# Optimization experiments

Measured on AMD Instinct MI355X. Metric: run time of the kernel, lower is better.

The kernel has to match this reference:

```python
import jax, jax.numpy as jnp
import numpy as np

H = 16          # num_heads
DK = 64         # k_dim_head
DV = 64         # v_dim_head
DIM = 1024      # model dim (= H*DK = H*DV)


def _split_heads(x, h):
    # ... T (H d) -> ... H T d
    x = x.reshape(x.shape[:-1] + (h, -1))
    return jnp.swapaxes(x, -2, -3)


def _merge_heads(x):
    # ... H T d -> ... T (H d)
    x = jnp.swapaxes(x, -2, -3)
    return x.reshape(x.shape[:-2] + (-1,))


def setup_inputs() -> dict:
    key = jax.random.key(0)
    ks = jax.random.split(key, 8)
    B, T = 2, 2048
    q = jax.random.normal(ks[0], (B, T, DIM), dtype=jnp.float32)
    k = jax.random.normal(ks[1], (B, T, DIM), dtype=jnp.float32)
    v = jax.random.normal(ks[2], (B, T, DIM), dtype=jnp.float32)
    # causal boolean mask [T, T] (True = attend)
    mask = jnp.tril(jnp.ones((T, T), dtype=bool))
    s = 1.0 / np.sqrt(DIM)
    # weights stored as [in, out] so projection is x @ W (== torch Linear, no bias)
    Wq = jax.random.normal(ks[3], (DIM, H * DK), dtype=jnp.float32) * s
    Wk = jax.random.normal(ks[4], (DIM, H * DK), dtype=jnp.float32) * s
    Wv = jax.random.normal(ks[5], (DIM, H * DV), dtype=jnp.float32) * s
    Wo = jax.random.normal(ks[6], (H * DV, DIM), dtype=jnp.float32) * s
    return {"q": q, "k": k, "v": v, "mask": mask,
            "Wq": Wq, "Wk": Wk, "Wv": Wv, "Wo": Wo}


def reference(q, k, v, mask, Wq, Wk, Wv, Wo):
    q_i = _split_heads(q @ Wq, H)                       # ... H T dk
    k_i = _split_heads(k @ Wk, H)                       # ... H T dk
    v_i = _split_heads(v @ Wv, H)                       # ... H T dv
    s_qk = jnp.einsum('...hik,...hjk->...hij', q_i, k_i) / jnp.sqrt(
        jnp.asarray(DK, dtype=q_i.dtype))               # ... H T T
    neg = -jnp.finfo(s_qk.dtype).max
    s_qk = jnp.where(mask, s_qk, neg)
    attn = jax.nn.softmax(s_qk, axis=-1)
    vals = jnp.einsum('...hij,...hjv->...hiv', attn, v_i)
    return _merge_heads(vals) @ Wo                      # ... T out_dim
```

## Files before the change

### kernel.cpp

```cpp
#include <hip/hip_runtime.h>
#include <hip/hip_bf16.h>
#include <stdint.h>

#define T_SEQ  2048
#define DMODEL 1024
#define NBATCH 2
#define NHEAD  16
#define DHEAD  64
#define MTOT   (NBATCH * T_SEQ)

typedef __attribute__((ext_vector_type(8))) short short8_t;
typedef __attribute__((ext_vector_type(4))) float f32x4;
typedef __attribute__((ext_vector_type(16))) float f32x16;
typedef __attribute__((ext_vector_type(2))) __bf16 bhalf2_t;
typedef __attribute__((ext_vector_type(4))) uint32_t uint4_t;

typedef const __attribute__((address_space(1))) void* gas_t;
typedef __attribute__((address_space(3))) void* las_t;

__device__ __forceinline__ ushort f2bf(float f) {
    return __builtin_bit_cast(unsigned short, (__bf16)f);
}
__device__ __forceinline__ uint32_t pk_bf16(float a, float b) {
    bhalf2_t t; t[0] = (__bf16)a; t[1] = (__bf16)b;
    return __builtin_bit_cast(uint32_t, t);
}

template <int B>
__device__ __forceinline__ short8_t pack8(const f32x16 &s) {
    uint4_t u;
    u[0] = pk_bf16(s[B + 0], s[B + 1]);
    u[1] = pk_bf16(s[B + 2], s[B + 3]);
    u[2] = pk_bf16(s[B + 4], s[B + 5]);
    u[3] = pk_bf16(s[B + 6], s[B + 7]);
    return __builtin_bit_cast(short8_t, u);
}

__global__ __launch_bounds__(256) void convert_qkv_kernel(
        const float* __restrict__ q, const float* __restrict__ k,
        const float* __restrict__ v, ushort* __restrict__ outb) {
    const size_t per = (size_t)MTOT * DMODEL / 4;
    size_t idx = (size_t)blockIdx.x * 256 + threadIdx.x;
    int t = (int)(idx / per);
    size_t i = idx - (size_t)t * per;
    const float4* src = (const float4*)(t == 0 ? q : (t == 1 ? k : v));
    float4 val = src[i];
    uint2 o;
    o.x = pk_bf16(val.x, val.y);
    o.y = pk_bf16(val.z, val.w);
    ((uint2*)outb)[(size_t)t * per + i] = o;
}

__global__ __launch_bounds__(256) void convw_kernel(
        const float* __restrict__ Wq, const float* __restrict__ Wk,
        const float* __restrict__ Wv, const float* __restrict__ Wo,
        ushort* __restrict__ wt) {
    __shared__ float tile[32][33];
    int z = blockIdx.z;
    const float* W = z == 0 ? Wq : z == 1 ? Wk : z == 2 ? Wv : Wo;
    const float sc = (z == 0) ? 0.18033688011f : 1.0f;
    ushort* out = wt + (size_t)z * DMODEL * DMODEL;
    int tx = threadIdx.x, ty = threadIdx.y;
    int k0 = blockIdx.x * 32, n0 = blockIdx.y * 32;
    #pragma unroll
    for (int i = 0; i < 4; i++)
        tile[ty + i * 8][tx] = W[(size_t)(k0 + ty + i * 8) * DMODEL + n0 + tx];
    __syncthreads();
    #pragma unroll
    for (int i = 0; i < 4; i++)
        out[(size_t)(n0 + ty + i * 8) * DMODEL + k0 + tx] = f2bf(tile[tx][ty + i * 8] * sc);
}

template <bool OUT_F32>
__global__ __launch_bounds__(256, 2) void gemm_bt_kernel(
        const ushort* __restrict__ Aall, const ushort* __restrict__ Btall,
        void* __restrict__ Call, int M, int N, int K) {
    const ushort* A  = Aall  + (size_t)blockIdx.z * M * K;
    const ushort* Bt = Btall + (size_t)blockIdx.z * N * K;

    __shared__ ushort As[128 * 32];
    __shared__ ushort Bs[128 * 32];

    const int tid  = threadIdx.x;
    const int lane = tid & 63;
    const int wid  = tid >> 6;
    const int wr = wid >> 1, wc = wid & 1;
    const int m_base = blockIdx.x * 128;
    const int n_base = blockIdx.y * 128;

    f32x4 acc[4][4] = {};

    const int srow = lane >> 2;
    const int scol = (lane & 3) * 8;

    for (int kk = 0; kk < K; kk += 32) {
        __syncthreads();
        #pragma unroll
        for (int i = 0; i < 2; i++) {
            int c = wid * 2 + i;
            const ushort* ga = A  + (size_t)(m_base + c * 16 + srow) * K + kk + scol;
            const ushort* gb = Bt + (size_t)(n_base + c * 16 + srow) * K + kk + scol;
            __builtin_amdgcn_global_load_lds((gas_t)ga, (las_t)(As + c * 512), 16, 0, 0);
            __builtin_amdgcn_global_load_lds((gas_t)gb, (las_t)(Bs + c * 512), 16, 0, 0);
        }
        __syncthreads();
        short8_t a[4], b[4];
        #pragma unroll
        for (int mt = 0; mt < 4; mt++)
            a[mt] = *(const short8_t*)(As + (wr * 64 + mt * 16 + (lane & 15)) * 32 + (lane >> 4) * 8);
        #pragma unroll
        for (int nt = 0; nt < 4; nt++)
            b[nt] = *(const short8_t*)(Bs + (wc * 64 + nt * 16 + (lane & 15)) * 32 + (lane >> 4) * 8);
        #pragma unroll
        for (int mt = 0; mt < 4; mt++)
            #pragma unroll
            for (int nt = 0; nt < 4; nt++)
                acc[mt][nt] = __builtin_amdgcn_mfma_f32_16x16x32_bf16(a[mt], b[nt], acc[mt][nt], 0, 0, 0);
    }

    const int row0 = m_base + wr * 64 + (lane >> 4) * 4;
    const int col0 = n_base + wc * 64 + (lane & 15);
    if constexpr (OUT_F32) {
        float* C = (float*)Call + (size_t)blockIdx.z * M * N;
        #pragma unroll
        for (int mt = 0; mt < 4; mt++)
            #pragma unroll
            for (int nt = 0; nt < 4; nt++)
                #pragma unroll
                for (int r = 0; r < 4; r++)
                    C[(size_t)(row0 + mt * 16 + r) * N + col0 + nt * 16] = acc[mt][nt][r];
    } else {
        ushort* C = (ushort*)Call + (size_t)blockIdx.z * M * N;
        #pragma unroll
        for (int mt = 0; mt < 4; mt++)
            #pragma unroll
            for (int nt = 0; nt < 4; nt++)
                #pragma unroll
                for (int r = 0; r < 4; r++)
                    C[(size_t)(row0 + mt * 16 + r) * N + col0 + nt * 16] = f2bf(acc[mt][nt][r]);
    }
}

__global__ __launch_bounds__(128, 2) void attn_kernel(
        const ushort* __restrict__ Qp, const ushort* __restrict__ Kp,
        const ushort* __restrict__ Vp, ushort* __restrict__ Op) {
    __shared__ __attribute__((aligned(16))) ushort Ksh[2][64 * 72];
    __shared__ __attribute__((aligned(16))) ushort Vts[2][64 * 72];

    const int tid = threadIdx.x, lane = tid & 63, w = tid >> 6;
    const int m31 = lane & 31, hi = lane >> 5;
    const int bh = blockIdx.y;
    const int b = bh >> 4, h = bh & 15;

    const ushort* Qb = Qp + (size_t)(b * T_SEQ) * DMODEL + h * DHEAD;
    const ushort* Kb = Kp + (size_t)(b * T_SEQ) * DMODEL + h * DHEAD;
    const ushort* Vb = Vp + (size_t)(b * T_SEQ) * DMODEL + h * DHEAD;
    ushort* Ob = Op + (size_t)(b * T_SEQ) * DMODEL + h * DHEAD;

    const int qi = 31 - (int)blockIdx.x;
    const int nt = qi + 1;
    const int q0 = qi * 64;
    const int q0w = q0 + w * 32;
    const int qg = q0w + m31;

    const int kr = tid >> 1, kc64 = (tid & 1) * 32;
    const int kvp = tid & 31, dvs = tid >> 5;
    const int lp = kvp & 7, q2 = lp >> 1;
    const int q2p = ((q2 & 1) << 1) | (q2 >> 1);
    const int kvc = (kvp & ~7) | (q2p << 1) | (lp & 1);

    short8_t kreg[4], vreg[4];
    auto LOADKV = [&](int kv0) {
        #pragma unroll
        for (int j = 0; j < 4; j++)
            kreg[j] = *(const short8_t*)(Kb + (size_t)(kv0 + kr) * DMODEL + kc64 + j * 8);
        const ushort* vsrc = Vb + (size_t)(kv0 + kvp * 2) * DMODEL + dvs * 16;
        vreg[0] = *(const short8_t*)(vsrc);
        vreg[1] = *(const short8_t*)(vsrc + 8);
        vreg[2] = *(const short8_t*)(vsrc + DMODEL);
        vreg[3] = *(const short8_t*)(vsrc + DMODEL + 8);
    };
    auto WRITEKV = [&](int buf) {
        #pragma unroll
        for (int j = 0; j < 4; j++)
            *(short8_t*)(&Ksh[buf][kr * 72 + kc64 + j * 8]) = kreg[j];
        #pragma unroll
        for (int c = 0; c < 2; c++) {
            uint4_t a = __builtin_bit_cast(uint4_t, vreg[c]);
            uint4_t o = __builtin_bit_cast(uint4_t, vreg[2 + c]);
            #pragma unroll
            for (int j = 0; j < 4; j++) {
                int d0 = dvs * 16 + c * 8 + 2 * j;
                *(uint32_t*)(&Vts[buf][(d0 + 0) * 72 + kvc * 2]) =
                    __builtin_amdgcn_perm(o[j], a[j], 0x05040100u);
                *(uint32_t*)(&Vts[buf][(d0 + 1) * 72 + kvc * 2]) =
                    __builtin_amdgcn_perm(o[j], a[j], 0x07060302u);
            }
        }
    };

    short8_t qf[4];
    #pragma unroll
    for (int dkc = 0; dkc < 4; dkc++)
        qf[dkc] = *(const short8_t*)(Qb + (size_t)(q0w + m31) * DMODEL + dkc * 16 + hi * 8);

    f32x16 acc0 = {}, acc1 = {};
    float mrun = -1e30f, lrun = 0.f;

    LOADKV(0);
    WRITEKV(0);
    LOADKV(64);

    for (int t = 0; t < nt; ++t) {
        const int kv0 = t * 64;
        const int cur = t & 1;
        const bool need_mask = (t == nt - 1);

        __syncthreads();
        if (t + 1 < nt) {
            WRITEKV(cur ^ 1);
            if (t + 2 < nt) LOADKV((t + 2) * 64);
        }

        f32x16 s0 = {}, s1 = {};
        __builtin_amdgcn_s_setprio(1);
        #pragma unroll
        for (int dkc = 0; dkc < 4; dkc++) {
            short8_t kf0 = *(const short8_t*)(&Ksh[cur][(m31) * 72 + dkc * 16 + hi * 8]);
            short8_t kf1 = *(const short8_t*)(&Ksh[cur][(32 + m31) * 72 + dkc * 16 + hi * 8]);
            s0 = __builtin_amdgcn_mfma_f32_32x32x16_bf16(kf0, qf[dkc], s0, 0, 0, 0);
            s1 = __builtin_amdgcn_mfma_f32_32x32x16_bf16(kf1, qf[dkc], s1, 0, 0, 0);
        }
        __builtin_amdgcn_s_setprio(0);

        if (need_mask) {
            const int kvb = kv0 + 4 * hi;
            #pragma unroll
            for (int r = 0; r < 16; r++) {
                int kvl = (r & 3) + 8 * (r >> 2);
                if (kvb + kvl      > qg) s0[r] = -1e30f;
                if (kvb + kvl + 32 > qg) s1[r] = -1e30f;
            }
        }

        float tm[16];
        #pragma unroll
        for (int r = 0; r < 16; r++) tm[r] = fmaxf(s0[r], s1[r]);
        #pragma unroll
        for (int st = 8; st >= 1; st >>= 1)
            #pragma unroll
            for (int i = 0; i < st; i++) tm[i] = fmaxf(tm[i], tm[i + st]);
        float pmax = fmaxf(tm[0], __shfl_xor(tm[0], 32));

        if (!__all(pmax <= mrun + 8.f)) {
            float mnew = fmaxf(mrun, pmax);
            float fac = exp2f(mrun - mnew);
            mrun = mnew;
            lrun *= fac;
            #pragma unroll
            for (int r = 0; r < 16; r++) {
                float fr = __shfl(fac, (r & 3) + 8 * (r >> 2) + 4 * hi);
                acc0[r] *= fr; acc1[r] *= fr;
            }
        }

        float ps[16];
        #pragma unroll
        for (int r = 0; r < 16; r++) {
            s0[r] = exp2f(s0[r] - mrun);
            s1[r] = exp2f(s1[r] - mrun);
            ps[r] = s0[r] + s1[r];
        }
        #pragma unroll
        for (int st = 8; st >= 1; st >>= 1)
            #pragma unroll
            for (int i = 0; i < st; i++) ps[i] += ps[i + st];
        lrun += ps[0] + __shfl_xor(ps[0], 32);

        short8_t pa[4];
        pa[0] = pack8<0>(s0);
        pa[1] = pack8<8>(s0);
        pa[2] = pack8<0>(s1);
        pa[3] = pack8<8>(s1);
        __builtin_amdgcn_s_setprio(1);
        #pragma unroll
        for (int ks = 0; ks < 4; ks++) {
            short8_t vf0 = *(const short8_t*)(&Vts[cur][(m31) * 72 + ks * 16 + hi * 8]);
            short8_t vf1 = *(const short8_t*)(&Vts[cur][(32 + m31) * 72 + ks * 16 + hi * 8]);
            acc0 = __builtin_amdgcn_mfma_f32_32x32x16_bf16(pa[ks], vf0, acc0, 0, 0, 0);
            acc1 = __builtin_amdgcn_mfma_f32_32x32x16_bf16(pa[ks], vf1, acc1, 0, 0, 0);
        }
        __builtin_amdgcn_s_setprio(0);
    }

    float linv = __builtin_amdgcn_rcpf(lrun);
    #pragma unroll
    for (int r = 0; r < 16; r++) {
        int ql = (r & 3) + 8 * (r >> 2) + 4 * hi;
        float li = __shfl(linv, ql);
        ushort* orow = Ob + (size_t)(q0w + ql) * DMODEL + m31;
        orow[0]  = f2bf(acc0[r] * li);
        orow[32] = f2bf(acc1[r] * li);
    }
}

extern "C" void kernel_launch(void* const* d_in, const int* in_sizes, int n_in,
                              void* d_out, int out_size, void* d_ws, size_t ws_size,
                              hipStream_t stream) {
    (void)in_sizes; (void)n_in; (void)out_size; (void)ws_size;
    const float* q  = (const float*)d_in[0];
    const float* k  = (const float*)d_in[1];
    const float* v  = (const float*)d_in[2];
    const float* Wq = (const float*)d_in[4];
    const float* Wk = (const float*)d_in[5];
    const float* Wv = (const float*)d_in[6];
    const float* Wo = (const float*)d_in[7];

    ushort* ws = (ushort*)d_ws;
    const size_t MK = (size_t)MTOT * DMODEL;
    const size_t NK = (size_t)DMODEL * DMODEL;
    ushort* qkvb = ws;
    ushort* wt   = ws + 3 * MK;
    ushort* qkvp = ws + 3 * MK + 4 * NK;
    ushort* Op   = ws;

    convert_qkv_kernel<<<dim3(12288), dim3(256), 0, stream>>>(q, k, v, qkvb);
    convw_kernel<<<dim3(32, 32, 4), dim3(32, 8), 0, stream>>>(Wq, Wk, Wv, Wo, wt);
    gemm_bt_kernel<false><<<dim3(32, 8, 3), dim3(256), 0, stream>>>(qkvb, wt, (void*)qkvp,
                                                                    MTOT, DMODEL, DMODEL);
    attn_kernel<<<dim3(32, 32), dim3(128), 0, stream>>>(qkvp, qkvp + MK, qkvp + 2 * MK, Op);
    gemm_bt_kernel<true><<<dim3(32, 8, 1), dim3(256), 0, stream>>>(Op, wt + 3 * NK, d_out,
                                                                   MTOT, DMODEL, DMODEL);
}
```

Before: 149.2 us.

## Pair causal query tiles per block to balance attention workload

Each attention block now handles two query tiles, qa and 31-qa, back to back, so every block processes exactly 33 KV tiles instead of a varying 1 to 32. The grid shrinks from 32x32 to 16x32 blocks, and the KV prefetch pipeline continues across the switch between the two query tiles. This targets the tail imbalance of causal attention, where blocks with many KV tiles finish late. In exchange there are half as many blocks to fill the GPU (512 blocks of 128 threads), plus an extra Q reload and output write in the middle of the loop.

```diff
diff --git a/kernel.cpp b/kernel.cpp
--- a/kernel.cpp
+++ b/kernel.cpp
@@ -157,11 +157,8 @@
     const ushort* Vb = Vp + (size_t)(b * T_SEQ) * DMODEL + h * DHEAD;
     ushort* Ob = Op + (size_t)(b * T_SEQ) * DMODEL + h * DHEAD;
 
-    const int qi = 31 - (int)blockIdx.x;
-    const int nt = qi + 1;
-    const int q0 = qi * 64;
-    const int q0w = q0 + w * 32;
-    const int qg = q0w + m31;
+    const int qa = blockIdx.x;
+    const int na = qa + 1;
 
     const int kr = tid >> 1, kc64 = (tid & 1) * 32;
     const int kvp = tid & 31, dvs = tid >> 5;
@@ -199,6 +196,7 @@
         }
     };
 
+    int qi = qa, q0w = qi * 64 + w * 32, qg = q0w + m31;
     short8_t qf[4];
     #pragma unroll
     for (int dkc = 0; dkc < 4; dkc++)
@@ -207,19 +205,42 @@
     f32x16 acc0 = {}, acc1 = {};
     float mrun = -1e30f, lrun = 0.f;
 
-    LOADKV(0);
+    auto WRITE_O = [&]() {
+        float linv = __builtin_amdgcn_rcpf(lrun);
+        #pragma unroll
+        for (int r = 0; r < 16; r++) {
+            int ql = (r & 3) + 8 * (r >> 2) + 4 * hi;
+            float li = __shfl(linv, ql);
+            ushort* orow = Ob + (size_t)(q0w + ql) * DMODEL + m31;
+            orow[0]  = f2bf(acc0[r] * li);
+            orow[32] = f2bf(acc1[r] * li);
+        }
+    };
+    auto TILE = [&](int t) { return (t < na) ? t : t - na; };
+
+    LOADKV(TILE(0) * 64);
     WRITEKV(0);
-    LOADKV(64);
-
-    for (int t = 0; t < nt; ++t) {
+    LOADKV(TILE(1) * 64);
+
+    for (int tt = 0; tt < 33; ++tt) {
+        if (tt == na) {
+            WRITE_O();
+            acc0 = f32x16{}; acc1 = f32x16{};
+            mrun = -1e30f; lrun = 0.f;
+            qi = 31 - qa; q0w = qi * 64 + w * 32; qg = q0w + m31;
+            #pragma unroll
+            for (int dkc = 0; dkc < 4; dkc++)
+                qf[dkc] = *(const short8_t*)(Qb + (size_t)(q0w + m31) * DMODEL + dkc * 16 + hi * 8);
+        }
+        const int t = TILE(tt);
         const int kv0 = t * 64;
-        const int cur = t & 1;
-        const bool need_mask = (t == nt - 1);
+        const int cur = tt & 1;
+        const bool need_mask = (t == qi);
 
         __syncthreads();
-        if (t + 1 < nt) {
+        if (tt + 1 < 33) {
             WRITEKV(cur ^ 1);
-            if (t + 2 < nt) LOADKV((t + 2) * 64);
+            if (tt + 2 < 33) LOADKV(TILE(tt + 2) * 64);
         }
 
         f32x16 s0 = {}, s1 = {};
@@ -292,16 +313,7 @@
         }
         __builtin_amdgcn_s_setprio(0);
     }
-
-    float linv = __builtin_amdgcn_rcpf(lrun);
-    #pragma unroll
-    for (int r = 0; r < 16; r++) {
-        int ql = (r & 3) + 8 * (r >> 2) + 4 * hi;
-        float li = __shfl(linv, ql);
-        ushort* orow = Ob + (size_t)(q0w + ql) * DMODEL + m31;
-        orow[0]  = f2bf(acc0[r] * li);
-        orow[32] = f2bf(acc1[r] * li);
-    }
+    WRITE_O();
 }
 
 extern "C" void kernel_launch(void* const* d_in, const int* in_sizes, int n_in,
@@ -328,7 +340,7 @@
     convw_kernel<<<dim3(32, 32, 4), dim3(32, 8), 0, stream>>>(Wq, Wk, Wv, Wo, wt);
     gemm_bt_kernel<false><<<dim3(32, 8, 3), dim3(256), 0, stream>>>(qkvb, wt, (void*)qkvp,
                                                                     MTOT, DMODEL, DMODEL);
-    attn_kernel<<<dim3(32, 32), dim3(128), 0, stream>>>(qkvp, qkvp + MK, qkvp + 2 * MK, Op);
+    attn_kernel<<<dim3(16, 32), dim3(128), 0, stream>>>(qkvp, qkvp + MK, qkvp + 2 * MK, Op);
     gemm_bt_kernel<true><<<dim3(32, 8, 1), dim3(256), 0, stream>>>(Op, wt + 3 * NK, d_out,
                                                                    MTOT, DMODEL, DMODEL);
 }
```

After: 146.2 us. -2.0%, faster.

## Split attention into single-wave blocks with balanced causal scheduling

Applied to the files above, without the earlier changes.

The attention kernel changes from 128-thread blocks (two waves sharing a 64-row query tile) to 64-thread single-wave blocks, each owning 32 query rows, for 2048 blocks. Block ids map to query tiles so consecutive blocks pair short and long causal rows, balancing work. Since only one wave uses the shared tiles, the LDS double buffer and __syncthreads are dropped: the next K/V tile is loaded into registers during compute and written to LDS after the PV MFMAs. In exchange, each wave loads full K/V tiles on its own, doubling global and LDS traffic per query row, and register pressure rises.

```diff
diff --git a/kernel.cpp b/kernel.cpp
--- a/kernel.cpp
+++ b/kernel.cpp
@@ -141,15 +141,20 @@
     }
 }
 
-__global__ __launch_bounds__(128, 2) void attn_kernel(
+__global__ __launch_bounds__(64, 2) void attn_kernel(
         const ushort* __restrict__ Qp, const ushort* __restrict__ Kp,
         const ushort* __restrict__ Vp, ushort* __restrict__ Op) {
-    __shared__ __attribute__((aligned(16))) ushort Ksh[2][64 * 72];
-    __shared__ __attribute__((aligned(16))) ushort Vts[2][64 * 72];
-
-    const int tid = threadIdx.x, lane = tid & 63, w = tid >> 6;
+    __shared__ __attribute__((aligned(16))) ushort Ksh[64 * 72];
+    __shared__ __attribute__((aligned(16))) ushort Vts[64 * 72];
+
+    const int lane = threadIdx.x;
     const int m31 = lane & 31, hi = lane >> 5;
-    const int bh = blockIdx.y;
+
+    const int id = (int)blockIdx.x;
+    const int low = id & 255, k8 = id >> 8;
+    const int bh = low >> 3;
+    const int u = ((k8 >> 1) << 3) | (low & 7);
+    const int qb = (k8 & 1) ? 63 - u : u;
     const int b = bh >> 4, h = bh & 15;
 
     const ushort* Qb = Qp + (size_t)(b * T_SEQ) * DMODEL + h * DHEAD;
@@ -157,44 +162,43 @@
     const ushort* Vb = Vp + (size_t)(b * T_SEQ) * DMODEL + h * DHEAD;
     ushort* Ob = Op + (size_t)(b * T_SEQ) * DMODEL + h * DHEAD;
 
-    const int qi = 31 - (int)blockIdx.x;
-    const int nt = qi + 1;
-    const int q0 = qi * 64;
-    const int q0w = q0 + w * 32;
+    const int nt = (qb >> 1) + 1;
+    const int q0w = qb * 32;
     const int qg = q0w + m31;
 
-    const int kr = tid >> 1, kc64 = (tid & 1) * 32;
-    const int kvp = tid & 31, dvs = tid >> 5;
+    const int kr8 = lane >> 3, kc8 = (lane & 7) * 8;
+    const int kvp = lane & 31, dvh = lane >> 5;
     const int lp = kvp & 7, q2 = lp >> 1;
     const int q2p = ((q2 & 1) << 1) | (q2 >> 1);
     const int kvc = (kvp & ~7) | (q2p << 1) | (lp & 1);
 
-    short8_t kreg[4], vreg[4];
+    short8_t kreg[8], vreg[8];
     auto LOADKV = [&](int kv0) {
         #pragma unroll
-        for (int j = 0; j < 4; j++)
-            kreg[j] = *(const short8_t*)(Kb + (size_t)(kv0 + kr) * DMODEL + kc64 + j * 8);
-        const ushort* vsrc = Vb + (size_t)(kv0 + kvp * 2) * DMODEL + dvs * 16;
-        vreg[0] = *(const short8_t*)(vsrc);
-        vreg[1] = *(const short8_t*)(vsrc + 8);
-        vreg[2] = *(const short8_t*)(vsrc + DMODEL);
-        vreg[3] = *(const short8_t*)(vsrc + DMODEL + 8);
+        for (int i = 0; i < 8; i++)
+            kreg[i] = *(const short8_t*)(Kb + (size_t)(kv0 + kr8 + 8 * i) * DMODEL + kc8);
+        const ushort* vsrc = Vb + (size_t)(kv0 + 2 * kvp) * DMODEL + dvh * 32;
+        #pragma unroll
+        for (int j = 0; j < 4; j++) {
+            vreg[j]     = *(const short8_t*)(vsrc + j * 8);
+            vreg[4 + j] = *(const short8_t*)(vsrc + DMODEL + j * 8);
+        }
     };
-    auto WRITEKV = [&](int buf) {
-        #pragma unroll
-        for (int j = 0; j < 4; j++)
-            *(short8_t*)(&Ksh[buf][kr * 72 + kc64 + j * 8]) = kreg[j];
-        #pragma unroll
-        for (int c = 0; c < 2; c++) {
-            uint4_t a = __builtin_bit_cast(uint4_t, vreg[c]);
-            uint4_t o = __builtin_bit_cast(uint4_t, vreg[2 + c]);
-            #pragma unroll
-            for (int j = 0; j < 4; j++) {
-                int d0 = dvs * 16 + c * 8 + 2 * j;
-                *(uint32_t*)(&Vts[buf][(d0 + 0) * 72 + kvc * 2]) =
-                    __builtin_amdgcn_perm(o[j], a[j], 0x05040100u);
-                *(uint32_t*)(&Vts[buf][(d0 + 1) * 72 + kvc * 2]) =
-                    __builtin_amdgcn_perm(o[j], a[j], 0x07060302u);
+    auto WRITEKV = [&]() {
+        #pragma unroll
+        for (int i = 0; i < 8; i++)
+            *(short8_t*)(&Ksh[(kr8 + 8 * i) * 72 + kc8]) = kreg[i];
+        #pragma unroll
+        for (int j = 0; j < 4; j++) {
+            uint4_t a = __builtin_bit_cast(uint4_t, vreg[j]);
+            uint4_t o = __builtin_bit_cast(uint4_t, vreg[4 + j]);
+            #pragma unroll
+            for (int jj = 0; jj < 4; jj++) {
+                int d0 = dvh * 32 + j * 8 + 2 * jj;
+                *(uint32_t*)(&Vts[(d0 + 0) * 72 + kvc * 2]) =
+                    __builtin_amdgcn_perm(o[jj], a[jj], 0x05040100u);
+                *(uint32_t*)(&Vts[(d0 + 1) * 72 + kvc * 2]) =
+                    __builtin_amdgcn_perm(o[jj], a[jj], 0x07060302u);
             }
         }
     };
@@ -208,26 +212,20 @@
     float mrun = -1e30f, lrun = 0.f;
 
     LOADKV(0);
-    WRITEKV(0);
-    LOADKV(64);
+    WRITEKV();
 
     for (int t = 0; t < nt; ++t) {
         const int kv0 = t * 64;
-        const int cur = t & 1;
         const bool need_mask = (t == nt - 1);
 
-        __syncthreads();
-        if (t + 1 < nt) {
-            WRITEKV(cur ^ 1);
-            if (t + 2 < nt) LOADKV((t + 2) * 64);
-        }
+        if (t + 1 < nt) LOADKV((t + 1) * 64);
 
         f32x16 s0 = {}, s1 = {};
         __builtin_amdgcn_s_setprio(1);
         #pragma unroll
         for (int dkc = 0; dkc < 4; dkc++) {
-            short8_t kf0 = *(const short8_t*)(&Ksh[cur][(m31) * 72 + dkc * 16 + hi * 8]);
-            short8_t kf1 = *(const short8_t*)(&Ksh[cur][(32 + m31) * 72 + dkc * 16 + hi * 8]);
+            short8_t kf0 = *(const short8_t*)(&Ksh[(m31) * 72 + dkc * 16 + hi * 8]);
+            short8_t kf1 = *(const short8_t*)(&Ksh[(32 + m31) * 72 + dkc * 16 + hi * 8]);
             s0 = __builtin_amdgcn_mfma_f32_32x32x16_bf16(kf0, qf[dkc], s0, 0, 0, 0);
             s1 = __builtin_amdgcn_mfma_f32_32x32x16_bf16(kf1, qf[dkc], s1, 0, 0, 0);
         }
@@ -285,12 +283,14 @@
         __builtin_amdgcn_s_setprio(1);
         #pragma unroll
         for (int ks = 0; ks < 4; ks++) {
-            short8_t vf0 = *(const short8_t*)(&Vts[cur][(m31) * 72 + ks * 16 + hi * 8]);
-            short8_t vf1 = *(const short8_t*)(&Vts[cur][(32 + m31) * 72 + ks * 16 + hi * 8]);
+            short8_t vf0 = *(const short8_t*)(&Vts[(m31) * 72 + ks * 16 + hi * 8]);
+            short8_t vf1 = *(const short8_t*)(&Vts[(32 + m31) * 72 + ks * 16 + hi * 8]);
             acc0 = __builtin_amdgcn_mfma_f32_32x32x16_bf16(pa[ks], vf0, acc0, 0, 0, 0);
             acc1 = __builtin_amdgcn_mfma_f32_32x32x16_bf16(pa[ks], vf1, acc1, 0, 0, 0);
         }
         __builtin_amdgcn_s_setprio(0);
+
+        if (t + 1 < nt) WRITEKV();
     }
 
     float linv = __builtin_amdgcn_rcpf(lrun);
@@ -328,7 +328,7 @@
     convw_kernel<<<dim3(32, 32, 4), dim3(32, 8), 0, stream>>>(Wq, Wk, Wv, Wo, wt);
     gemm_bt_kernel<false><<<dim3(32, 8, 3), dim3(256), 0, stream>>>(qkvb, wt, (void*)qkvp,
                                                                     MTOT, DMODEL, DMODEL);
-    attn_kernel<<<dim3(32, 32), dim3(128), 0, stream>>>(qkvp, qkvp + MK, qkvp + 2 * MK, Op);
+    attn_kernel<<<dim3(2048), dim3(64), 0, stream>>>(qkvp, qkvp + MK, qkvp + 2 * MK, Op);
     gemm_bt_kernel<true><<<dim3(32, 8, 1), dim3(256), 0, stream>>>(Op, wt + 3 * NK, d_out,
                                                                    MTOT, DMODEL, DMODEL);
 }
```

After: 148.1 us. Within noise of the previous version (-0.7%).

## Use 128-row query tiles with 4 waves and atomic work-queue scheduling in attention

Applied to the files above, without the earlier changes.

Attention blocks now process 128 query rows with four waves sharing each K/V shared-memory tile, halving global K/V traffic per query. Blocks fetch work units from an atomic counter in largest-first order to balance the causal triangle, and a small kernel resets the counter. Waves whose rows end before the last tile skip compute on that tile but still take part in the loads and barriers. The cost is one more launch and some idle wave time on the diagonal tiles.

```diff
diff --git a/kernel.cpp b/kernel.cpp
--- a/kernel.cpp
+++ b/kernel.cpp
@@ -71,6 +71,10 @@
         out[(size_t)(n0 + ty + i * 8) * DMODEL + k0 + tx] = f2bf(tile[tx][ty + i * 8] * sc);
 }
 
+__global__ void zero_ctr_kernel(uint32_t* ctr) {
+    if (threadIdx.x == 0 && blockIdx.x == 0) *ctr = 0u;
+}
+
 template <bool OUT_F32>
 __global__ __launch_bounds__(256, 2) void gemm_bt_kernel(
         const ushort* __restrict__ Aall, const ushort* __restrict__ Btall,
@@ -141,166 +145,169 @@
     }
 }
 
-__global__ __launch_bounds__(128, 2) void attn_kernel(
+__global__ __launch_bounds__(256, 2) void attn_kernel(
         const ushort* __restrict__ Qp, const ushort* __restrict__ Kp,
-        const ushort* __restrict__ Vp, ushort* __restrict__ Op) {
+        const ushort* __restrict__ Vp, ushort* __restrict__ Op,
+        uint32_t* __restrict__ ctr) {
     __shared__ __attribute__((aligned(16))) ushort Ksh[2][64 * 72];
     __shared__ __attribute__((aligned(16))) ushort Vts[2][64 * 72];
+    __shared__ int unit_j;
 
     const int tid = threadIdx.x, lane = tid & 63, w = tid >> 6;
     const int m31 = lane & 31, hi = lane >> 5;
-    const int bh = blockIdx.y;
-    const int b = bh >> 4, h = bh & 15;
-
-    const ushort* Qb = Qp + (size_t)(b * T_SEQ) * DMODEL + h * DHEAD;
-    const ushort* Kb = Kp + (size_t)(b * T_SEQ) * DMODEL + h * DHEAD;
-    const ushort* Vb = Vp + (size_t)(b * T_SEQ) * DMODEL + h * DHEAD;
-    ushort* Ob = Op + (size_t)(b * T_SEQ) * DMODEL + h * DHEAD;
-
-    const int qi = 31 - (int)blockIdx.x;
-    const int nt = qi + 1;
-    const int q0 = qi * 64;
-    const int q0w = q0 + w * 32;
-    const int qg = q0w + m31;
-
-    const int kr = tid >> 1, kc64 = (tid & 1) * 32;
-    const int kvp = tid & 31, dvs = tid >> 5;
+
+    const int kr  = tid >> 3, kck = (tid & 7) * 8;
+    const int kvp = tid & 31, dvc = tid >> 5;
     const int lp = kvp & 7, q2 = lp >> 1;
     const int q2p = ((q2 & 1) << 1) | (q2 >> 1);
     const int kvc = (kvp & ~7) | (q2p << 1) | (lp & 1);
 
-    short8_t kreg[4], vreg[4];
+    const ushort *Qb, *Kb, *Vb;
+    ushort *Ob;
+    short8_t kreg0, kreg1, vreg0, vreg1;
     auto LOADKV = [&](int kv0) {
-        #pragma unroll
-        for (int j = 0; j < 4; j++)
-            kreg[j] = *(const short8_t*)(Kb + (size_t)(kv0 + kr) * DMODEL + kc64 + j * 8);
-        const ushort* vsrc = Vb + (size_t)(kv0 + kvp * 2) * DMODEL + dvs * 16;
-        vreg[0] = *(const short8_t*)(vsrc);
-        vreg[1] = *(const short8_t*)(vsrc + 8);
-        vreg[2] = *(const short8_t*)(vsrc + DMODEL);
-        vreg[3] = *(const short8_t*)(vsrc + DMODEL + 8);
+        kreg0 = *(const short8_t*)(Kb + (size_t)(kv0 + kr) * DMODEL + kck);
+        kreg1 = *(const short8_t*)(Kb + (size_t)(kv0 + kr + 32) * DMODEL + kck);
+        const ushort* vsrc = Vb + (size_t)(kv0 + kvp * 2) * DMODEL + dvc * 8;
+        vreg0 = *(const short8_t*)(vsrc);
+        vreg1 = *(const short8_t*)(vsrc + DMODEL);
     };
     auto WRITEKV = [&](int buf) {
-        #pragma unroll
-        for (int j = 0; j < 4; j++)
-            *(short8_t*)(&Ksh[buf][kr * 72 + kc64 + j * 8]) = kreg[j];
-        #pragma unroll
-        for (int c = 0; c < 2; c++) {
-            uint4_t a = __builtin_bit_cast(uint4_t, vreg[c]);
-            uint4_t o = __builtin_bit_cast(uint4_t, vreg[2 + c]);
-            #pragma unroll
-            for (int j = 0; j < 4; j++) {
-                int d0 = dvs * 16 + c * 8 + 2 * j;
-                *(uint32_t*)(&Vts[buf][(d0 + 0) * 72 + kvc * 2]) =
-                    __builtin_amdgcn_perm(o[j], a[j], 0x05040100u);
-                *(uint32_t*)(&Vts[buf][(d0 + 1) * 72 + kvc * 2]) =
-                    __builtin_amdgcn_perm(o[j], a[j], 0x07060302u);
+        *(short8_t*)(&Ksh[buf][kr * 72 + kck]) = kreg0;
+        *(short8_t*)(&Ksh[buf][(kr + 32) * 72 + kck]) = kreg1;
+        uint4_t a = __builtin_bit_cast(uint4_t, vreg0);
+        uint4_t o = __builtin_bit_cast(uint4_t, vreg1);
+        #pragma unroll
+        for (int j = 0; j < 4; j++) {
+            *(uint32_t*)(&Vts[buf][(dvc * 8 + 2 * j) * 72 + kvc * 2]) =
+                __builtin_amdgcn_perm(o[j], a[j], 0x05040100u);
+            *(uint32_t*)(&Vts[buf][(dvc * 8 + 2 * j + 1) * 72 + kvc * 2]) =
+                __builtin_amdgcn_perm(o[j], a[j], 0x07060302u);
+        }
+    };
+
+    for (;;) {
+        __syncthreads();
+        if (tid == 0) unit_j = (int)atomicAdd(ctr, 1u);
+        __syncthreads();
+        const int j = unit_j;
+        if (j >= 512) break;
+
+        const int qa = 15 - (j >> 5);
+        const int bh = j & 31;
+        const int b = bh >> 4, h = bh & 15;
+        Qb = Qp + (size_t)(b * T_SEQ) * DMODEL + h * DHEAD;
+        Kb = Kp + (size_t)(b * T_SEQ) * DMODEL + h * DHEAD;
+        Vb = Vp + (size_t)(b * T_SEQ) * DMODEL + h * DHEAD;
+        Ob = Op + (size_t)(b * T_SEQ) * DMODEL + h * DHEAD;
+
+        const int ntile = 2 * qa + 2;
+        const int q0w = qa * 128 + w * 32;
+        const int qg = q0w + m31;
+        const int diag = 2 * qa + (w >> 1);
+
+        short8_t qf[4];
+        #pragma unroll
+        for (int dkc = 0; dkc < 4; dkc++)
+            qf[dkc] = *(const short8_t*)(Qb + (size_t)(q0w + m31) * DMODEL + dkc * 16 + hi * 8);
+
+        f32x16 acc0 = {}, acc1 = {};
+        float mrun = -1e30f, lrun = 0.f;
+
+        LOADKV(0);
+        WRITEKV(0);
+        LOADKV(64);
+
+        for (int tt = 0; tt < ntile; ++tt) {
+            const int cur = tt & 1;
+            __syncthreads();
+            if (tt + 1 < ntile) {
+                WRITEKV(cur ^ 1);
+                if (tt + 2 < ntile) LOADKV((tt + 2) * 64);
+            }
+
+            if (tt <= diag) {
+                const int kv0 = tt * 64;
+                f32x16 s0 = {}, s1 = {};
+                __builtin_amdgcn_s_setprio(1);
+                #pragma unroll
+                for (int dkc = 0; dkc < 4; dkc++) {
+                    short8_t kf0 = *(const short8_t*)(&Ksh[cur][(m31) * 72 + dkc * 16 + hi * 8]);
+                    short8_t kf1 = *(const short8_t*)(&Ksh[cur][(32 + m31) * 72 + dkc * 16 + hi * 8]);
+                    s0 = __builtin_amdgcn_mfma_f32_32x32x16_bf16(kf0, qf[dkc], s0, 0, 0, 0);
+                    s1 = __builtin_amdgcn_mfma_f32_32x32x16_bf16(kf1, qf[dkc], s1, 0, 0, 0);
+                }
+                __builtin_amdgcn_s_setprio(0);
+
+                if (tt == diag) {
+                    const int kvb = kv0 + 4 * hi;
+                    #pragma unroll
+                    for (int r = 0; r < 16; r++) {
+                        int kvl = (r & 3) + 8 * (r >> 2);
+                        if (kvb + kvl      > qg) s0[r] = -1e30f;
+                        if (kvb + kvl + 32 > qg) s1[r] = -1e30f;
+                    }
+                }
+
+                float tm[16];
+                #pragma unroll
+                for (int r = 0; r < 16; r++) tm[r] = fmaxf(s0[r], s1[r]);
+                #pragma unroll
+                for (int st = 8; st >= 1; st >>= 1)
+                    #pragma unroll
+                    for (int i = 0; i < st; i++) tm[i] = fmaxf(tm[i], tm[i + st]);
+                float pmax = fmaxf(tm[0], __shfl_xor(tm[0], 32));
+
+                if (!__all(pmax <= mrun + 8.f)) {
+                    float mnew = fmaxf(mrun, pmax);
+                    float fac = exp2f(mrun - mnew);
+                    mrun = mnew;
+                    lrun *= fac;
+                    #pragma unroll
+                    for (int r = 0; r < 16; r++) {
+                        float fr = __shfl(fac, (r & 3) + 8 * (r >> 2) + 4 * hi);
+                        acc0[r] *= fr; acc1[r] *= fr;
+                    }
+                }
+                float ps[16];
+                #pragma unroll
+                for (int r = 0; r < 16; r++) {
+                    s0[r] = exp2f(s0[r] - mrun);
+                    s1[r] = exp2f(s1[r] - mrun);
+                    ps[r] = s0[r] + s1[r];
+                }
+                #pragma unroll
+                for (int st = 8; st >= 1; st >>= 1)
+                    #pragma unroll
+                    for (int i = 0; i < st; i++) ps[i] += ps[i + st];
+                lrun += ps[0] + __shfl_xor(ps[0], 32);
+
+                short8_t pa[4];
+                pa[0] = pack8<0>(s0);
+                pa[1] = pack8<8>(s0);
+                pa[2] = pack8<0>(s1);
+                pa[3] = pack8<8>(s1);
+                __builtin_amdgcn_s_setprio(1);
+                #pragma unroll
+                for (int ks = 0; ks < 4; ks++) {
+                    short8_t vf0 = *(const short8_t*)(&Vts[cur][(m31) * 72 + ks * 16 + hi * 8]);
+                    short8_t vf1 = *(const short8_t*)(&Vts[cur][(32 + m31) * 72 + ks * 16 + hi * 8]);
+                    acc0 = __builtin_amdgcn_mfma_f32_32x32x16_bf16(pa[ks], vf0, acc0, 0, 0, 0);
+                    acc1 = __builtin_amdgcn_mfma_f32_32x32x16_bf16(pa[ks], vf1, acc1, 0, 0, 0);
+                }
+                __builtin_amdgcn_s_setprio(0);
             }
         }
-    };
-
-    short8_t qf[4];
-    #pragma unroll
-    for (int dkc = 0; dkc < 4; dkc++)
-        qf[dkc] = *(const short8_t*)(Qb + (size_t)(q0w + m31) * DMODEL + dkc * 16 + hi * 8);
-
-    f32x16 acc0 = {}, acc1 = {};
-    float mrun = -1e30f, lrun = 0.f;
-
-    LOADKV(0);
-    WRITEKV(0);
-    LOADKV(64);
-
-    for (int t = 0; t < nt; ++t) {
-        const int kv0 = t * 64;
-        const int cur = t & 1;
-        const bool need_mask = (t == nt - 1);
-
-        __syncthreads();
-        if (t + 1 < nt) {
-            WRITEKV(cur ^ 1);
-            if (t + 2 < nt) LOADKV((t + 2) * 64);
+
+        float linv = __builtin_amdgcn_rcpf(lrun);
+        #pragma unroll
+        for (int r = 0; r < 16; r++) {
+            int ql = (r & 3) + 8 * (r >> 2) + 4 * hi;
+            float li = __shfl(linv, ql);
+            ushort* orow = Ob + (size_t)(q0w + ql) * DMODEL + m31;
+            orow[0]  = f2bf(acc0[r] * li);
+            orow[32] = f2bf(acc1[r] * li);
         }
-
-        f32x16 s0 = {}, s1 = {};
-        __builtin_amdgcn_s_setprio(1);
-        #pragma unroll
-        for (int dkc = 0; dkc < 4; dkc++) {
-            short8_t kf0 = *(const short8_t*)(&Ksh[cur][(m31) * 72 + dkc * 16 + hi * 8]);
-            short8_t kf1 = *(const short8_t*)(&Ksh[cur][(32 + m31) * 72 + dkc * 16 + hi * 8]);
-            s0 = __builtin_amdgcn_mfma_f32_32x32x16_bf16(kf0, qf[dkc], s0, 0, 0, 0);
-            s1 = __builtin_amdgcn_mfma_f32_32x32x16_bf16(kf1, qf[dkc], s1, 0, 0, 0);
-        }
-        __builtin_amdgcn_s_setprio(0);
-
-        if (need_mask) {
-            const int kvb = kv0 + 4 * hi;
-            #pragma unroll
-            for (int r = 0; r < 16; r++) {
-                int kvl = (r & 3) + 8 * (r >> 2);
-                if (kvb + kvl      > qg) s0[r] = -1e30f;
-                if (kvb + kvl + 32 > qg) s1[r] = -1e30f;
-            }
-        }
-
-        float tm[16];
-        #pragma unroll
-        for (int r = 0; r < 16; r++) tm[r] = fmaxf(s0[r], s1[r]);
-        #pragma unroll
-        for (int st = 8; st >= 1; st >>= 1)
-            #pragma unroll
-            for (int i = 0; i < st; i++) tm[i] = fmaxf(tm[i], tm[i + st]);
-        float pmax = fmaxf(tm[0], __shfl_xor(tm[0], 32));
-
-        if (!__all(pmax <= mrun + 8.f)) {
-            float mnew = fmaxf(mrun, pmax);
-            float fac = exp2f(mrun - mnew);
-            mrun = mnew;
-            lrun *= fac;
-            #pragma unroll
-            for (int r = 0; r < 16; r++) {
-                float fr = __shfl(fac, (r & 3) + 8 * (r >> 2) + 4 * hi);
-                acc0[r] *= fr; acc1[r] *= fr;
-            }
-        }
-
-        float ps[16];
-        #pragma unroll
-        for (int r = 0; r < 16; r++) {
-            s0[r] = exp2f(s0[r] - mrun);
-            s1[r] = exp2f(s1[r] - mrun);
-            ps[r] = s0[r] + s1[r];
-        }
-        #pragma unroll
-        for (int st = 8; st >= 1; st >>= 1)
-            #pragma unroll
-            for (int i = 0; i < st; i++) ps[i] += ps[i + st];
-        lrun += ps[0] + __shfl_xor(ps[0], 32);
-
-        short8_t pa[4];
-        pa[0] = pack8<0>(s0);
-        pa[1] = pack8<8>(s0);
-        pa[2] = pack8<0>(s1);
-        pa[3] = pack8<8>(s1);
-        __builtin_amdgcn_s_setprio(1);
-        #pragma unroll
-        for (int ks = 0; ks < 4; ks++) {
-            short8_t vf0 = *(const short8_t*)(&Vts[cur][(m31) * 72 + ks * 16 + hi * 8]);
-            short8_t vf1 = *(const short8_t*)(&Vts[cur][(32 + m31) * 72 + ks * 16 + hi * 8]);
-            acc0 = __builtin_amdgcn_mfma_f32_32x32x16_bf16(pa[ks], vf0, acc0, 0, 0, 0);
-            acc1 = __builtin_amdgcn_mfma_f32_32x32x16_bf16(pa[ks], vf1, acc1, 0, 0, 0);
-        }
-        __builtin_amdgcn_s_setprio(0);
-    }
-
-    float linv = __builtin_amdgcn_rcpf(lrun);
-    #pragma unroll
-    for (int r = 0; r < 16; r++) {
-        int ql = (r & 3) + 8 * (r >> 2) + 4 * hi;
-        float li = __shfl(linv, ql);
-        ushort* orow = Ob + (size_t)(q0w + ql) * DMODEL + m31;
-        orow[0]  = f2bf(acc0[r] * li);
-        orow[32] = f2bf(acc1[r] * li);
     }
 }
 
@@ -323,12 +330,14 @@
     ushort* wt   = ws + 3 * MK;
     ushort* qkvp = ws + 3 * MK + 4 * NK;
     ushort* Op   = ws;
+    uint32_t* ctr = (uint32_t*)(ws + 3 * MK + 4 * NK + 3 * MK);
 
     convert_qkv_kernel<<<dim3(12288), dim3(256), 0, stream>>>(q, k, v, qkvb);
     convw_kernel<<<dim3(32, 32, 4), dim3(32, 8), 0, stream>>>(Wq, Wk, Wv, Wo, wt);
+    zero_ctr_kernel<<<dim3(1), dim3(64), 0, stream>>>(ctr);
     gemm_bt_kernel<false><<<dim3(32, 8, 3), dim3(256), 0, stream>>>(qkvb, wt, (void*)qkvp,
                                                                     MTOT, DMODEL, DMODEL);
-    attn_kernel<<<dim3(32, 32), dim3(128), 0, stream>>>(qkvp, qkvp + MK, qkvp + 2 * MK, Op);
+    attn_kernel<<<dim3(512), dim3(256), 0, stream>>>(qkvp, qkvp + MK, qkvp + 2 * MK, Op, ctr);
     gemm_bt_kernel<true><<<dim3(32, 8, 1), dim3(256), 0, stream>>>(Op, wt + 3 * NK, d_out,
                                                                    MTOT, DMODEL, DMODEL);
 }
```

Result: faster. 145.1 us (-2.7%).
